# Kernel optimization log

Measured on AMD Instinct MI355X. Metric: run time of the kernel, lower is better.

The kernel has to match this reference:

```python
import jax, jax.numpy as jnp
import numpy as np

IN_F = 4096
OUT_F = 4096
ORDER = 8
N_ROWS = 8192


def setup_inputs() -> dict:
    key = jax.random.key(0)
    ks = jax.random.split(key, 10)
    maxf = max(IN_F, OUT_F)
    minf = min(IN_F, OUT_F)
    return {
        "x": jax.random.normal(ks[0], (N_ROWS, IN_F), jnp.float32),
        "v_mean": jax.random.normal(ks[1], (ORDER, maxf), jnp.float32),
        "v_logvar": jax.random.normal(ks[2], (ORDER, maxf), jnp.float32) - 5.0,
        "d_mean": jax.random.normal(ks[3], (minf,), jnp.float32),
        "d_logvar": jax.random.normal(ks[4], (minf,), jnp.float32) - 5.0,
        "bias_mean": jax.random.normal(ks[5], (OUT_F,), jnp.float32) * 0.01,
        "bias_logvar": jax.random.normal(ks[6], (OUT_F,), jnp.float32) * 0.01 - 5.0,
        "eps_v": jax.random.normal(ks[7], (ORDER, maxf), jnp.float32),
        "eps_d": jax.random.normal(ks[8], (minf,), jnp.float32),
        "eps_b": jax.random.normal(ks[9], (OUT_F,), jnp.float32),
    }


def _householder_chain(v_normed, dtype):
    # Product H_0 @ H_1 @ ... @ H_{k-1}, H_i = I - 2 v_i v_i^T, via rank-1 updates:
    # P @ H_i = P - 2 (P v_i) v_i^T  -- mathematically identical to the dense
    # eye-expand + mm chain in the torch module, O(order*F^2) instead of O(order*F^3).
    maxf = v_normed.shape[1]

    def step(P, vi):
        Pv = P @ vi                      # [F]
        return P - 2.0 * Pv[:, None] * vi[None, :], None

    u, _ = jax.lax.scan(step, jnp.eye(maxf, dtype=dtype), v_normed)
    return u


def reference(x, v_mean, v_logvar, d_mean, d_logvar, bias_mean, bias_logvar,
              eps_v, eps_d, eps_b):
    # Reparameterized samples
    v = v_mean + jnp.exp(0.5 * v_logvar) * eps_v        # [order, maxF]
    d = d_mean + jnp.exp(0.5 * d_logvar) * eps_d        # [minF]
    bias = bias_mean + jnp.exp(0.5 * bias_logvar) * eps_b  # [out]

    vn = v / jnp.linalg.norm(v, axis=1, keepdims=True)
    u = _householder_chain(vn, x.dtype)                 # [maxF, maxF] orthogonal

    if OUT_F <= IN_F:
        # W = u @ eye(in,out) @ diag(d) == first OUT_F cols of u, scaled by d
        W = u[:, :OUT_F] * d[None, :]                   # [in, out]
    else:
        # W = diag(d) @ eye(in,out) @ u == first IN_F rows of u, scaled by d
        W = d[:, None] * u[:IN_F, :]                    # [in, out]

    return x @ W + bias[None, :]
```

## Files before the change

kernel.cpp:

```cpp
#include <hip/hip_runtime.h>

#define ORDER 8
#define FDIM 4096
#define NROWS 8192
#define THREADS 256
#define RPB 4
#define F4T 4
#define F4DIM (FDIM/4)
#define NPAIR 36

__global__ __launch_bounds__(THREADS) void obd_prep(
    const float* __restrict__ v_mean, const float* __restrict__ v_logvar,
    const float* __restrict__ eps_v,
    const float* __restrict__ d_mean, const float* __restrict__ d_logvar,
    const float* __restrict__ eps_d,
    const float* __restrict__ b_mean, const float* __restrict__ b_logvar,
    const float* __restrict__ eps_b,
    float* __restrict__ vn, float* __restrict__ dsc, float* __restrict__ bias)
{
    const int b = blockIdx.x;
    const int t = threadIdx.x;
    __shared__ float red[THREADS / 64];

    if (b < ORDER) {
        const float4* vm = (const float4*)(v_mean   + (size_t)b * FDIM);
        const float4* vl = (const float4*)(v_logvar + (size_t)b * FDIM);
        const float4* ev = (const float4*)(eps_v    + (size_t)b * FDIM);
        float4 val[F4T];
        float ss = 0.f;
        #pragma unroll
        for (int k = 0; k < F4T; ++k) {
            const int idx = t + k * THREADS;
            float4 m = vm[idx], l = vl[idx], e = ev[idx];
            float4 v;
            v.x = fmaf(expf(0.5f * l.x), e.x, m.x);
            v.y = fmaf(expf(0.5f * l.y), e.y, m.y);
            v.z = fmaf(expf(0.5f * l.z), e.z, m.z);
            v.w = fmaf(expf(0.5f * l.w), e.w, m.w);
            val[k] = v;
            ss += v.x * v.x + v.y * v.y + v.z * v.z + v.w * v.w;
        }
        #pragma unroll
        for (int off = 32; off; off >>= 1) ss += __shfl_down(ss, off);
        const int wave = t >> 6, lane = t & 63;
        if (lane == 0) red[wave] = ss;
        __syncthreads();
        const float inv = 1.0f / sqrtf(red[0] + red[1] + red[2] + red[3]);
        float4* vno = (float4*)(vn + (size_t)b * FDIM);
        #pragma unroll
        for (int k = 0; k < F4T; ++k) {
            const int idx = t + k * THREADS;
            float4 v = val[k];
            v.x *= inv; v.y *= inv; v.z *= inv; v.w *= inv;
            vno[idx] = v;
        }
    } else if (b == ORDER) {
        #pragma unroll
        for (int k = 0; k < 16; ++k) {
            const int idx = t + k * THREADS;
            dsc[idx] = fmaf(expf(0.5f * d_logvar[idx]), eps_d[idx], d_mean[idx]);
        }
    } else {
        #pragma unroll
        for (int k = 0; k < 16; ++k) {
            const int idx = t + k * THREADS;
            bias[idx] = fmaf(expf(0.5f * b_logvar[idx]), eps_b[idx], b_mean[idx]);
        }
    }
}

__global__ __launch_bounds__(THREADS) void obd_gramT(
    const float* __restrict__ vn, float* __restrict__ Tm)
{
    const int t = threadIdx.x;
    const int wave = t >> 6, lane = t & 63;
    const float4* Vv = (const float4*)vn;

    float acc[ORDER][ORDER];
    #pragma unroll
    for (int i = 0; i < ORDER; ++i)
        #pragma unroll
        for (int j = i; j < ORDER; ++j) acc[i][j] = 0.f;

    #pragma unroll
    for (int k = 0; k < F4T; ++k) {
        const int idx = t + k * THREADS;
        float4 vc[ORDER];
        #pragma unroll
        for (int i = 0; i < ORDER; ++i) vc[i] = Vv[i * F4DIM + idx];
        #pragma unroll
        for (int i = 0; i < ORDER; ++i)
            #pragma unroll
            for (int j = i; j < ORDER; ++j) {
                acc[i][j] = fmaf(vc[i].x, vc[j].x, acc[i][j]);
                acc[i][j] = fmaf(vc[i].y, vc[j].y, acc[i][j]);
                acc[i][j] = fmaf(vc[i].z, vc[j].z, acc[i][j]);
                acc[i][j] = fmaf(vc[i].w, vc[j].w, acc[i][j]);
            }
    }
    #pragma unroll
    for (int off = 32; off; off >>= 1)
        #pragma unroll
        for (int i = 0; i < ORDER; ++i)
            #pragma unroll
            for (int j = i; j < ORDER; ++j)
                acc[i][j] += __shfl_down(acc[i][j], off);

    __shared__ float red[THREADS / 64][NPAIR];
    if (lane == 0) {
        int p = 0;
        #pragma unroll
        for (int i = 0; i < ORDER; ++i)
            #pragma unroll
            for (int j = i; j < ORDER; ++j) red[wave][p++] = acc[i][j];
    }
    __syncthreads();
    if (t == 0) {
        float G[ORDER][ORDER];
        int p = 0;
        for (int i = 0; i < ORDER; ++i)
            for (int j = i; j < ORDER; ++j) {
                G[i][j] = red[0][p] + red[1][p] + red[2][p] + red[3][p];
                ++p;
            }
        float T[ORDER][ORDER];
        for (int i = 0; i < ORDER; ++i)
            for (int j = 0; j < ORDER; ++j) T[i][j] = 0.f;
        T[0][0] = 2.f;
        for (int j = 1; j < ORDER; ++j) {
            for (int i = 0; i < j; ++i) {
                float s = 0.f;
                for (int m = i; m < j; ++m) s += T[i][m] * G[m][j];
                T[i][j] = -2.f * s;
            }
            T[j][j] = 2.f;
        }
        for (int i = 0; i < ORDER; ++i)
            for (int j = 0; j < ORDER; ++j) Tm[i * ORDER + j] = T[i][j];
    }
}

__global__ __launch_bounds__(THREADS, 2) void obd_wy(
    const float* __restrict__ x, const float* __restrict__ vn,
    const float* __restrict__ Tm, const float* __restrict__ dsc,
    const float* __restrict__ bias, float* __restrict__ out)
{
    const int t = threadIdx.x;
    const int wave = t >> 6, lane = t & 63;
    const size_t row0 = (size_t)blockIdx.x * RPB;
    const float4* xv = (const float4*)x;
    const float4* Vv = (const float4*)vn;
    float4* ov = (float4*)out;

    __shared__ float Ts[64];
    __shared__ float red[THREADS / 64][RPB * ORDER];
    if (t < 64) Ts[t] = Tm[t];

    float4 r[RPB][F4T];
    #pragma unroll
    for (int rr = 0; rr < RPB; ++rr) {
        const size_t base = (row0 + rr) * F4DIM;
        #pragma unroll
        for (int k = 0; k < F4T; ++k)
            r[rr][k] = xv[base + t + k * THREADS];
    }

    float p[RPB][ORDER];
    #pragma unroll
    for (int rr = 0; rr < RPB; ++rr)
        #pragma unroll
        for (int i = 0; i < ORDER; ++i) p[rr][i] = 0.f;

    #pragma unroll
    for (int k = 0; k < F4T; ++k) {
        const int idx = t + k * THREADS;
        #pragma unroll
        for (int i = 0; i < ORDER; ++i) {
            const float4 vc = Vv[i * F4DIM + idx];
            #pragma unroll
            for (int rr = 0; rr < RPB; ++rr) {
                p[rr][i] = fmaf(r[rr][k].x, vc.x, p[rr][i]);
                p[rr][i] = fmaf(r[rr][k].y, vc.y, p[rr][i]);
                p[rr][i] = fmaf(r[rr][k].z, vc.z, p[rr][i]);
                p[rr][i] = fmaf(r[rr][k].w, vc.w, p[rr][i]);
            }
        }
    }
    #pragma unroll
    for (int off = 32; off; off >>= 1)
        #pragma unroll
        for (int rr = 0; rr < RPB; ++rr)
            #pragma unroll
            for (int i = 0; i < ORDER; ++i)
                p[rr][i] += __shfl_down(p[rr][i], off);
    if (lane == 0) {
        #pragma unroll
        for (int rr = 0; rr < RPB; ++rr)
            #pragma unroll
            for (int i = 0; i < ORDER; ++i)
                red[wave][rr * ORDER + i] = p[rr][i];
    }
    __syncthreads();

    float mq[RPB][ORDER];
    #pragma unroll
    for (int rr = 0; rr < RPB; ++rr) {
        float dot[ORDER];
        #pragma unroll
        for (int i = 0; i < ORDER; ++i)
            dot[i] = red[0][rr * ORDER + i] + red[1][rr * ORDER + i]
                   + red[2][rr * ORDER + i] + red[3][rr * ORDER + i];
        #pragma unroll
        for (int j = 0; j < ORDER; ++j) {
            float s = 0.f;
            #pragma unroll
            for (int i = 0; i <= j; ++i) s = fmaf(dot[i], Ts[i * ORDER + j], s);
            mq[rr][j] = -s;
        }
    }

    const float4* dv = (const float4*)dsc;
    const float4* bv = (const float4*)bias;
    #pragma unroll
    for (int k = 0; k < F4T; ++k) {
        const int idx = t + k * THREADS;
        #pragma unroll
        for (int i = 0; i < ORDER; ++i) {
            const float4 vc = Vv[i * F4DIM + idx];
            #pragma unroll
            for (int rr = 0; rr < RPB; ++rr) {
                r[rr][k].x = fmaf(mq[rr][i], vc.x, r[rr][k].x);
                r[rr][k].y = fmaf(mq[rr][i], vc.y, r[rr][k].y);
                r[rr][k].z = fmaf(mq[rr][i], vc.z, r[rr][k].z);
                r[rr][k].w = fmaf(mq[rr][i], vc.w, r[rr][k].w);
            }
        }
        const float4 dd = dv[idx];
        const float4 bb = bv[idx];
        #pragma unroll
        for (int rr = 0; rr < RPB; ++rr) {
            float4 o;
            o.x = fmaf(r[rr][k].x, dd.x, bb.x);
            o.y = fmaf(r[rr][k].y, dd.y, bb.y);
            o.z = fmaf(r[rr][k].z, dd.z, bb.z);
            o.w = fmaf(r[rr][k].w, dd.w, bb.w);
            ov[(row0 + rr) * F4DIM + idx] = o;
        }
    }
}

extern "C" void kernel_launch(void* const* d_in, const int* in_sizes, int n_in,
                              void* d_out, int out_size, void* d_ws, size_t ws_size,
                              hipStream_t stream) {
    const float* x        = (const float*)d_in[0];
    const float* v_mean   = (const float*)d_in[1];
    const float* v_logvar = (const float*)d_in[2];
    const float* d_mean   = (const float*)d_in[3];
    const float* d_logvar = (const float*)d_in[4];
    const float* b_mean   = (const float*)d_in[5];
    const float* b_logvar = (const float*)d_in[6];
    const float* eps_v    = (const float*)d_in[7];
    const float* eps_d    = (const float*)d_in[8];
    const float* eps_b    = (const float*)d_in[9];

    float* ws   = (float*)d_ws;
    float* vn   = ws;
    float* dsc  = ws + ORDER * FDIM;
    float* bias = ws + ORDER * FDIM + FDIM;
    float* Tm   = ws + ORDER * FDIM + 2 * FDIM;

    obd_prep<<<ORDER + 2, THREADS, 0, stream>>>(
        v_mean, v_logvar, eps_v, d_mean, d_logvar, eps_d,
        b_mean, b_logvar, eps_b, vn, dsc, bias);
    obd_gramT<<<1, THREADS, 0, stream>>>(vn, Tm);
    obd_wy<<<NROWS / RPB, THREADS, 0, stream>>>(
        x, vn, Tm, dsc, bias, (float*)d_out);
}
```

Baseline: 76.08 us.

## Re-read x in second WY pass instead of holding it in registers; nontemporal stores

Result: slower. 91.29 us (+20.0%).

```diff
diff --git a/kernel.cpp b/kernel.cpp
--- a/kernel.cpp
+++ b/kernel.cpp
@@ -8,6 +8,8 @@
 #define F4T 4
 #define F4DIM (FDIM/4)
 #define NPAIR 36
+
+typedef float fvec4 __attribute__((ext_vector_type(4)));
 
 __global__ __launch_bounds__(THREADS) void obd_prep(
     const float* __restrict__ v_mean, const float* __restrict__ v_logvar,
@@ -23,22 +25,21 @@
     __shared__ float red[THREADS / 64];
 
     if (b < ORDER) {
-        const float4* vm = (const float4*)(v_mean   + (size_t)b * FDIM);
-        const float4* vl = (const float4*)(v_logvar + (size_t)b * FDIM);
-        const float4* ev = (const float4*)(eps_v    + (size_t)b * FDIM);
-        float4 val[F4T];
+        const fvec4* vm = (const fvec4*)(v_mean   + (size_t)b * FDIM);
+        const fvec4* vl = (const fvec4*)(v_logvar + (size_t)b * FDIM);
+        const fvec4* ev = (const fvec4*)(eps_v    + (size_t)b * FDIM);
+        fvec4 val[F4T];
         float ss = 0.f;
         #pragma unroll
         for (int k = 0; k < F4T; ++k) {
             const int idx = t + k * THREADS;
-            float4 m = vm[idx], l = vl[idx], e = ev[idx];
-            float4 v;
-            v.x = fmaf(expf(0.5f * l.x), e.x, m.x);
-            v.y = fmaf(expf(0.5f * l.y), e.y, m.y);
-            v.z = fmaf(expf(0.5f * l.z), e.z, m.z);
-            v.w = fmaf(expf(0.5f * l.w), e.w, m.w);
+            fvec4 m = vm[idx], l = vl[idx], e = ev[idx];
+            fvec4 v;
+            #pragma unroll
+            for (int c = 0; c < 4; ++c)
+                v[c] = fmaf(expf(0.5f * l[c]), e[c], m[c]);
             val[k] = v;
-            ss += v.x * v.x + v.y * v.y + v.z * v.z + v.w * v.w;
+            ss += v[0]*v[0] + v[1]*v[1] + v[2]*v[2] + v[3]*v[3];
         }
         #pragma unroll
         for (int off = 32; off; off >>= 1) ss += __shfl_down(ss, off);
@@ -46,13 +47,11 @@
         if (lane == 0) red[wave] = ss;
         __syncthreads();
         const float inv = 1.0f / sqrtf(red[0] + red[1] + red[2] + red[3]);
-        float4* vno = (float4*)(vn + (size_t)b * FDIM);
+        fvec4* vno = (fvec4*)(vn + (size_t)b * FDIM);
         #pragma unroll
         for (int k = 0; k < F4T; ++k) {
             const int idx = t + k * THREADS;
-            float4 v = val[k];
-            v.x *= inv; v.y *= inv; v.z *= inv; v.w *= inv;
-            vno[idx] = v;
+            vno[idx] = val[k] * inv;
         }
     } else if (b == ORDER) {
         #pragma unroll
@@ -74,7 +73,7 @@
 {
     const int t = threadIdx.x;
     const int wave = t >> 6, lane = t & 63;
-    const float4* Vv = (const float4*)vn;
+    const fvec4* Vv = (const fvec4*)vn;
 
     float acc[ORDER][ORDER];
     #pragma unroll
@@ -85,18 +84,16 @@
     #pragma unroll
     for (int k = 0; k < F4T; ++k) {
         const int idx = t + k * THREADS;
-        float4 vc[ORDER];
+        fvec4 vc[ORDER];
         #pragma unroll
         for (int i = 0; i < ORDER; ++i) vc[i] = Vv[i * F4DIM + idx];
         #pragma unroll
         for (int i = 0; i < ORDER; ++i)
             #pragma unroll
-            for (int j = i; j < ORDER; ++j) {
-                acc[i][j] = fmaf(vc[i].x, vc[j].x, acc[i][j]);
-                acc[i][j] = fmaf(vc[i].y, vc[j].y, acc[i][j]);
-                acc[i][j] = fmaf(vc[i].z, vc[j].z, acc[i][j]);
-                acc[i][j] = fmaf(vc[i].w, vc[j].w, acc[i][j]);
-            }
+            for (int j = i; j < ORDER; ++j)
+                #pragma unroll
+                for (int c = 0; c < 4; ++c)
+                    acc[i][j] = fmaf(vc[i][c], vc[j][c], acc[i][j]);
     }
     #pragma unroll
     for (int off = 32; off; off >>= 1)
@@ -140,7 +137,7 @@
     }
 }
 
-__global__ __launch_bounds__(THREADS, 2) void obd_wy(
+__global__ __launch_bounds__(THREADS) void obd_wy(
     const float* __restrict__ x, const float* __restrict__ vn,
     const float* __restrict__ Tm, const float* __restrict__ dsc,
     const float* __restrict__ bias, float* __restrict__ out)
@@ -148,23 +145,14 @@
     const int t = threadIdx.x;
     const int wave = t >> 6, lane = t & 63;
     const size_t row0 = (size_t)blockIdx.x * RPB;
-    const float4* xv = (const float4*)x;
-    const float4* Vv = (const float4*)vn;
-    float4* ov = (float4*)out;
+    const fvec4* xv = (const fvec4*)x;
+    const fvec4* Vv = (const fvec4*)vn;
+    fvec4* ov = (fvec4*)out;
 
     __shared__ float Ts[64];
     __shared__ float red[THREADS / 64][RPB * ORDER];
     if (t < 64) Ts[t] = Tm[t];
 
-    float4 r[RPB][F4T];
-    #pragma unroll
-    for (int rr = 0; rr < RPB; ++rr) {
-        const size_t base = (row0 + rr) * F4DIM;
-        #pragma unroll
-        for (int k = 0; k < F4T; ++k)
-            r[rr][k] = xv[base + t + k * THREADS];
-    }
-
     float p[RPB][ORDER];
     #pragma unroll
     for (int rr = 0; rr < RPB; ++rr)
@@ -174,16 +162,18 @@
     #pragma unroll
     for (int k = 0; k < F4T; ++k) {
         const int idx = t + k * THREADS;
+        fvec4 xr[RPB];
+        #pragma unroll
+        for (int rr = 0; rr < RPB; ++rr)
+            xr[rr] = xv[(row0 + rr) * F4DIM + idx];
         #pragma unroll
         for (int i = 0; i < ORDER; ++i) {
-            const float4 vc = Vv[i * F4DIM + idx];
-            #pragma unroll
-            for (int rr = 0; rr < RPB; ++rr) {
-                p[rr][i] = fmaf(r[rr][k].x, vc.x, p[rr][i]);
-                p[rr][i] = fmaf(r[rr][k].y, vc.y, p[rr][i]);
-                p[rr][i] = fmaf(r[rr][k].z, vc.z, p[rr][i]);
-                p[rr][i] = fmaf(r[rr][k].w, vc.w, p[rr][i]);
-            }
+            const fvec4 vc = Vv[i * F4DIM + idx];
+            #pragma unroll
+            for (int rr = 0; rr < RPB; ++rr)
+                #pragma unroll
+                for (int c = 0; c < 4; ++c)
+                    p[rr][i] = fmaf(xr[rr][c], vc[c], p[rr][i]);
         }
     }
     #pragma unroll
@@ -219,32 +209,33 @@
         }
     }
 
-    const float4* dv = (const float4*)dsc;
-    const float4* bv = (const float4*)bias;
+    const fvec4* dv = (const fvec4*)dsc;
+    const fvec4* bv = (const fvec4*)bias;
     #pragma unroll
     for (int k = 0; k < F4T; ++k) {
         const int idx = t + k * THREADS;
+        fvec4 acc[RPB];
+        #pragma unroll
+        for (int rr = 0; rr < RPB; ++rr)
+            acc[rr] = xv[(row0 + rr) * F4DIM + idx];
         #pragma unroll
         for (int i = 0; i < ORDER; ++i) {
-            const float4 vc = Vv[i * F4DIM + idx];
-            #pragma unroll
-            for (int rr = 0; rr < RPB; ++rr) {
-                r[rr][k].x = fmaf(mq[rr][i], vc.x, r[rr][k].x);
-                r[rr][k].y = fmaf(mq[rr][i], vc.y, r[rr][k].y);
-                r[rr][k].z = fmaf(mq[rr][i], vc.z, r[rr][k].z);
-                r[rr][k].w = fmaf(mq[rr][i], vc.w, r[rr][k].w);
-            }
-        }
-        const float4 dd = dv[idx];
-        const float4 bb = bv[idx];
+            const fvec4 vc = Vv[i * F4DIM + idx];
+            #pragma unroll
+            for (int rr = 0; rr < RPB; ++rr)
+                #pragma unroll
+                for (int c = 0; c < 4; ++c)
+                    acc[rr][c] = fmaf(mq[rr][i], vc[c], acc[rr][c]);
+        }
+        const fvec4 dd = dv[idx];
+        const fvec4 bb = bv[idx];
         #pragma unroll
         for (int rr = 0; rr < RPB; ++rr) {
-            float4 o;
-            o.x = fmaf(r[rr][k].x, dd.x, bb.x);
-            o.y = fmaf(r[rr][k].y, dd.y, bb.y);
-            o.z = fmaf(r[rr][k].z, dd.z, bb.z);
-            o.w = fmaf(r[rr][k].w, dd.w, bb.w);
-            ov[(row0 + rr) * F4DIM + idx] = o;
+            fvec4 o;
+            #pragma unroll
+            for (int c = 0; c < 4; ++c)
+                o[c] = fmaf(acc[rr][c], dd[c], bb[c]);
+            __builtin_nontemporal_store(o, &ov[(row0 + rr) * F4DIM + idx]);
         }
     }
 }
```
